# Kernel optimization log

Hardware: AMD Instinct MI355X
Metric: run time of the kernel (lower is better)

Reference implementation:

```python
import jax, jax.numpy as jnp
import numpy as np

N, M, Z_DIM = 32768, 8192, 64


def setup_inputs() -> dict:
    key = jax.random.key(0)
    kz, ke = jax.random.split(key)
    z = jax.random.normal(kz, (N, Z_DIM), dtype=jnp.float32)
    # torch: e = rand(M, z_dim) * 2 - 1  -> uniform in [-1, 1)
    e = jax.random.uniform(ke, (M, Z_DIM), dtype=jnp.float32, minval=-1.0, maxval=1.0)
    return {"z": z, "e": e}


def reference(z, e):
    # data['z'] = tanh(z)
    zt = jnp.tanh(z)                                   # (N, Z)
    # pairwise squared distance via Gram expansion:
    # ||a - b||^2 = ||a||^2 + ||b||^2 - 2 a.b  (same math as the
    # broadcasted sum((a-b)**2) without the (N, M, Z) intermediate)
    zn = jnp.sum(zt * zt, axis=1)                      # (N,)
    en = jnp.sum(e * e, axis=1)                        # (M,)
    distance = zn[:, None] + en[None, :] - 2.0 * (zt @ e.T)   # (N, M)
    # min over the batch dim N for each sample e, then mean over M
    loss = jnp.mean(jnp.min(distance, axis=0))
    return loss
```

## Files before the change

kernel.cpp:

```cpp
#include <hip/hip_runtime.h>
#include <hip/hip_bf16.h>
#include <math.h>

#define NN 32768
#define MM 8192
#define ZD 64
#define WAVES 4
#define MW 128
#define MBLK (WAVES * MW)
#define NCHUNKS 32
#define CHUNK (NN / NCHUNKS)
#define NROWS 64
#define NITER (CHUNK / NROWS)

typedef __attribute__((ext_vector_type(8))) short bf16x8;
typedef __attribute__((ext_vector_type(4))) float f32x4;

__device__ inline unsigned short f2bf(float f) {
  unsigned u = __float_as_uint(f);
  return (unsigned short)((u + 0x7fffu + ((u >> 16) & 1u)) >> 16);
}
__device__ inline float bf2f(unsigned short h) {
  return __uint_as_float(((unsigned)h) << 16);
}

__global__ __launch_bounds__(256) void prep_z(const float* __restrict__ z,
                                              unsigned short* __restrict__ zb,
                                              float* __restrict__ zn) {
  const int row = blockIdx.x * 32 + (threadIdx.x >> 3);
  const int q = threadIdx.x & 7;
  const size_t base = (size_t)row * ZD + q * 8;
  float4 v0 = *reinterpret_cast<const float4*>(&z[base]);
  float4 v1 = *reinterpret_cast<const float4*>(&z[base + 4]);
  float in[8] = {v0.x, v0.y, v0.z, v0.w, v1.x, v1.y, v1.z, v1.w};
  unsigned short b[8];
  float s = 0.f;
#pragma unroll
  for (int i = 0; i < 8; ++i) {
    b[i] = f2bf(tanhf(in[i]));
    float r = bf2f(b[i]);
    s += r * r;
  }
  *reinterpret_cast<bf16x8*>(&zb[base]) = *reinterpret_cast<bf16x8*>(b);
  s += __shfl_xor(s, 1, 64);
  s += __shfl_xor(s, 2, 64);
  s += __shfl_xor(s, 4, 64);
  if (q == 0) zn[row] = s;
}

__global__ __launch_bounds__(256) void prep_e(const float* __restrict__ e,
                                              unsigned short* __restrict__ eb,
                                              float* __restrict__ en) {
  const int row = blockIdx.x * 32 + (threadIdx.x >> 3);
  const int q = threadIdx.x & 7;
  const size_t base = (size_t)row * ZD + q * 8;
  float4 v0 = *reinterpret_cast<const float4*>(&e[base]);
  float4 v1 = *reinterpret_cast<const float4*>(&e[base + 4]);
  float in[8] = {v0.x, v0.y, v0.z, v0.w, v1.x, v1.y, v1.z, v1.w};
  unsigned short b[8];
  float s = 0.f;
#pragma unroll
  for (int i = 0; i < 8; ++i) {
    unsigned short qb = f2bf(in[i]);
    float r = bf2f(qb);
    s += r * r;
    b[i] = f2bf(-2.f * r);
  }
  *reinterpret_cast<bf16x8*>(&eb[base]) = *reinterpret_cast<bf16x8*>(b);
  s += __shfl_xor(s, 1, 64);
  s += __shfl_xor(s, 2, 64);
  s += __shfl_xor(s, 4, 64);
  if (q == 0) en[row] = s;
}

__global__ __launch_bounds__(256) void min_dist(
    const unsigned short* __restrict__ zb, const unsigned short* __restrict__ eb,
    const float* __restrict__ zn, float* __restrict__ partial) {
  __shared__ __align__(128) unsigned short zlds[2][NROWS * ZD];
  const int lane = threadIdx.x & 63;
  const int wv = threadIdx.x >> 6;
  const int lr = lane & 15;
  const int lg = lane >> 4;
  const int m0 = blockIdx.x * MBLK + wv * MW;
  const int nb0 = blockIdx.y * CHUNK;

  const int srow = lane >> 3;
  const int sslot = (lane & 7) ^ srow;

  bf16x8 bfr[8][2];
#pragma unroll
  for (int t = 0; t < 8; ++t)
#pragma unroll
    for (int h = 0; h < 2; ++h)
      bfr[t][h] = *reinterpret_cast<const bf16x8*>(
          &eb[(size_t)(m0 + t * 16 + lr) * ZD + h * 32 + lg * 8]);

  f32x4 minv[8];
#pragma unroll
  for (int t = 0; t < 8; ++t)
    minv[t] = (f32x4){3.4e38f, 3.4e38f, 3.4e38f, 3.4e38f};

  auto stage = [&](int buf, int nb) {
#pragma unroll
    for (int j = 0; j < 2; ++j) {
      const int i = wv * 2 + j;
      const char* src = (const char*)zb +
          (size_t)(nb + i * 8 + srow) * 128 + (sslot << 4);
      char* dst = (char*)&zlds[buf][0] + i * 1024;
      __builtin_amdgcn_global_load_lds(
          (const __attribute__((address_space(1))) unsigned int*)src,
          (__attribute__((address_space(3))) unsigned int*)dst, 16, 0, 0);
    }
  };

  stage(0, nb0);
  __syncthreads();

  for (int it = 0; it < NITER; ++it) {
    const int buf = it & 1;
    if (it + 1 < NITER) stage(buf ^ 1, nb0 + (it + 1) * NROWS);
    const char* lbase = (const char*)&zlds[buf][0];
#pragma unroll
    for (int s = 0; s < 4; ++s) {
      const int rb = (s * 16 + lr) * 128;
      const int x0 = (lg * 16) ^ ((lr & 7) << 4);
      bf16x8 a0 = *reinterpret_cast<const bf16x8*>(lbase + rb + x0);
      bf16x8 a1 = *reinterpret_cast<const bf16x8*>(lbase + rb + (x0 ^ 64));
      f32x4 znv = *reinterpret_cast<const f32x4*>(
          &zn[nb0 + it * NROWS + s * 16 + lg * 4]);
#pragma unroll
      for (int t = 0; t < 8; ++t) {
        f32x4 acc = __builtin_amdgcn_mfma_f32_16x16x32_bf16(a0, bfr[t][0], znv, 0, 0, 0);
        acc = __builtin_amdgcn_mfma_f32_16x16x32_bf16(a1, bfr[t][1], acc, 0, 0, 0);
#pragma unroll
        for (int r = 0; r < 4; ++r) minv[t][r] = fminf(minv[t][r], acc[r]);
      }
    }
    __syncthreads();
  }

#pragma unroll
  for (int t = 0; t < 8; ++t) {
    float v = fminf(fminf(minv[t][0], minv[t][1]), fminf(minv[t][2], minv[t][3]));
    v = fminf(v, __shfl_xor(v, 16, 64));
    v = fminf(v, __shfl_xor(v, 32, 64));
    if (lg == 0) partial[(size_t)blockIdx.y * MM + m0 + t * 16 + lr] = v;
  }
}

__global__ __launch_bounds__(256) void finalize1(const float* __restrict__ partial,
                                                 const float* __restrict__ en,
                                                 double* __restrict__ bsum) {
  const int m = blockIdx.x * 256 + threadIdx.x;
  float mv = partial[m];
#pragma unroll
  for (int c = 1; c < NCHUNKS; ++c)
    mv = fminf(mv, partial[(size_t)c * MM + m]);
  double s = (double)(mv + en[m]);
  __shared__ double sred[256];
  sred[threadIdx.x] = s;
  __syncthreads();
  for (int off = 128; off > 0; off >>= 1) {
    if ((int)threadIdx.x < off) sred[threadIdx.x] += sred[threadIdx.x + off];
    __syncthreads();
  }
  if (threadIdx.x == 0) bsum[blockIdx.x] = sred[0];
}

__global__ __launch_bounds__(64) void finalize2(const double* __restrict__ bsum,
                                                float* __restrict__ out) {
  double s = (threadIdx.x < MM / 256) ? bsum[threadIdx.x] : 0.0;
  s += __shfl_xor(s, 1, 64);
  s += __shfl_xor(s, 2, 64);
  s += __shfl_xor(s, 4, 64);
  s += __shfl_xor(s, 8, 64);
  s += __shfl_xor(s, 16, 64);
  s += __shfl_xor(s, 32, 64);
  if (threadIdx.x == 0) out[0] = (float)(s / (double)MM);
}

extern "C" void kernel_launch(void* const* d_in, const int* in_sizes, int n_in,
                              void* d_out, int out_size, void* d_ws, size_t ws_size,
                              hipStream_t stream) {
  const float* z = (const float*)d_in[0];
  const float* e = (const float*)d_in[1];
  float* out = (float*)d_out;

  unsigned short* zb = (unsigned short*)d_ws;
  unsigned short* eb = zb + (size_t)NN * ZD;
  float* zn = (float*)(eb + (size_t)MM * ZD);
  float* en = zn + NN;
  float* partial = en + MM;
  double* bsum = (double*)(partial + (size_t)NCHUNKS * MM);

  prep_z<<<NN / 32, 256, 0, stream>>>(z, zb, zn);
  prep_e<<<MM / 32, 256, 0, stream>>>(e, eb, en);
  dim3 grid(MM / MBLK, NCHUNKS);
  min_dist<<<grid, 256, 0, stream>>>(zb, eb, zn, partial);
  finalize1<<<MM / 256, 256, 0, stream>>>(partial, en, bsum);
  finalize2<<<1, 64, 0, stream>>>(bsum, out);
}
```

Baseline: 55.25 us.

## Halve per-wave M tile, remap 1D grid across XCDs, add occupancy hint

Each wave now covers 64 columns of e instead of 128, so the grid doubles to 1024 workgroups with fewer registers per wave, and launch_bounds requests 4 blocks per CU. The 2D grid becomes 1D with a swizzle that spreads consecutive block IDs across the 8 XCDs while keeping same-chunk blocks together for L2 reuse of z. Staging addresses and zn pointers are precomputed and incremented instead of recomputed each iteration. The cost is that each z tile loaded into LDS feeds half as many MFMAs per wave, which doubles LDS staging traffic relative to compute.

```diff
diff --git a/kernel.cpp b/kernel.cpp
--- a/kernel.cpp
+++ b/kernel.cpp
@@ -6,8 +6,9 @@
 #define MM 8192
 #define ZD 64
 #define WAVES 4
-#define MW 128
+#define MW 64
 #define MBLK (WAVES * MW)
+#define NMB (MM / MBLK)
 #define NCHUNKS 32
 #define CHUNK (NN / NCHUNKS)
 #define NROWS 64
@@ -73,78 +74,86 @@
   if (q == 0) en[row] = s;
 }
 
-__global__ __launch_bounds__(256) void min_dist(
+__global__ __launch_bounds__(256, 4) void min_dist(
     const unsigned short* __restrict__ zb, const unsigned short* __restrict__ eb,
     const float* __restrict__ zn, float* __restrict__ partial) {
   __shared__ __align__(128) unsigned short zlds[2][NROWS * ZD];
+  const int wg = ((blockIdx.x & 7) << 7) + (blockIdx.x >> 3);
+  const int mb = wg & (NMB - 1);
+  const int cb = wg >> 5;
   const int lane = threadIdx.x & 63;
   const int wv = threadIdx.x >> 6;
   const int lr = lane & 15;
   const int lg = lane >> 4;
-  const int m0 = blockIdx.x * MBLK + wv * MW;
-  const int nb0 = blockIdx.y * CHUNK;
+  const int m0 = mb * MBLK + wv * MW;
+  const int nb0 = cb * CHUNK;
 
   const int srow = lane >> 3;
   const int sslot = (lane & 7) ^ srow;
-
-  bf16x8 bfr[8][2];
-#pragma unroll
-  for (int t = 0; t < 8; ++t)
+  const char* zsrc = (const char*)zb + (size_t)nb0 * 128 +
+                     (wv * 16 + srow) * 128 + (sslot << 4);
+  char* ldst0 = (char*)&zlds[0][0] + wv * 2048;
+  char* ldst1 = (char*)&zlds[1][0] + wv * 2048;
+
+  bf16x8 bfr[4][2];
+#pragma unroll
+  for (int t = 0; t < 4; ++t)
 #pragma unroll
     for (int h = 0; h < 2; ++h)
       bfr[t][h] = *reinterpret_cast<const bf16x8*>(
           &eb[(size_t)(m0 + t * 16 + lr) * ZD + h * 32 + lg * 8]);
 
-  f32x4 minv[8];
-#pragma unroll
-  for (int t = 0; t < 8; ++t)
+  f32x4 minv[4];
+#pragma unroll
+  for (int t = 0; t < 4; ++t)
     minv[t] = (f32x4){3.4e38f, 3.4e38f, 3.4e38f, 3.4e38f};
 
-  auto stage = [&](int buf, int nb) {
-#pragma unroll
-    for (int j = 0; j < 2; ++j) {
-      const int i = wv * 2 + j;
-      const char* src = (const char*)zb +
-          (size_t)(nb + i * 8 + srow) * 128 + (sslot << 4);
-      char* dst = (char*)&zlds[buf][0] + i * 1024;
-      __builtin_amdgcn_global_load_lds(
-          (const __attribute__((address_space(1))) unsigned int*)src,
-          (__attribute__((address_space(3))) unsigned int*)dst, 16, 0, 0);
+  auto stage = [&](char* dst, const char* src) {
+    __builtin_amdgcn_global_load_lds(
+        (const __attribute__((address_space(1))) unsigned int*)src,
+        (__attribute__((address_space(3))) unsigned int*)dst, 16, 0, 0);
+    __builtin_amdgcn_global_load_lds(
+        (const __attribute__((address_space(1))) unsigned int*)(src + 1024),
+        (__attribute__((address_space(3))) unsigned int*)(dst + 1024), 16, 0, 0);
+  };
+
+  const float* znp = zn + nb0;
+  const int x0 = (lg * 16) ^ ((lr & 7) << 4);
+
+  stage(ldst0, zsrc);
+  zsrc += 8192;
+  __syncthreads();
+
+  for (int it = 0; it < NITER; ++it) {
+    const char* lbase = (it & 1) ? (const char*)&zlds[1][0] : (const char*)&zlds[0][0];
+    if (it + 1 < NITER) {
+      stage((it & 1) ? ldst0 : ldst1, zsrc);
+      zsrc += 8192;
     }
-  };
-
-  stage(0, nb0);
-  __syncthreads();
-
-  for (int it = 0; it < NITER; ++it) {
-    const int buf = it & 1;
-    if (it + 1 < NITER) stage(buf ^ 1, nb0 + (it + 1) * NROWS);
-    const char* lbase = (const char*)&zlds[buf][0];
 #pragma unroll
     for (int s = 0; s < 4; ++s) {
       const int rb = (s * 16 + lr) * 128;
-      const int x0 = (lg * 16) ^ ((lr & 7) << 4);
       bf16x8 a0 = *reinterpret_cast<const bf16x8*>(lbase + rb + x0);
       bf16x8 a1 = *reinterpret_cast<const bf16x8*>(lbase + rb + (x0 ^ 64));
-      f32x4 znv = *reinterpret_cast<const f32x4*>(
-          &zn[nb0 + it * NROWS + s * 16 + lg * 4]);
-#pragma unroll
-      for (int t = 0; t < 8; ++t) {
+      f32x4 znv = *reinterpret_cast<const f32x4*>(znp + s * 16 + lg * 4);
+#pragma unroll
+      for (int t = 0; t < 4; ++t) {
         f32x4 acc = __builtin_amdgcn_mfma_f32_16x16x32_bf16(a0, bfr[t][0], znv, 0, 0, 0);
         acc = __builtin_amdgcn_mfma_f32_16x16x32_bf16(a1, bfr[t][1], acc, 0, 0, 0);
 #pragma unroll
         for (int r = 0; r < 4; ++r) minv[t][r] = fminf(minv[t][r], acc[r]);
       }
     }
+    znp += NROWS;
     __syncthreads();
   }
 
 #pragma unroll
-  for (int t = 0; t < 8; ++t) {
+  for (int t = 0; t < 4; ++t) {
     float v = fminf(fminf(minv[t][0], minv[t][1]), fminf(minv[t][2], minv[t][3]));
     v = fminf(v, __shfl_xor(v, 16, 64));
     v = fminf(v, __shfl_xor(v, 32, 64));
-    if (lg == 0) partial[(size_t)blockIdx.y * MM + m0 + t * 16 + lr] = v;
+    if (lg == 0) partial[(size_t)cb * MM + m0 + t * 16 + lr] = v;
   }
 }
 
@@ -195,8 +204,7 @@
 
   prep_z<<<NN / 32, 256, 0, stream>>>(z, zb, zn);
   prep_e<<<MM / 32, 256, 0, stream>>>(e, eb, en);
-  dim3 grid(MM / MBLK, NCHUNKS);
-  min_dist<<<grid, 256, 0, stream>>>(zb, eb, zn, partial);
+  min_dist<<<NMB * NCHUNKS, 256, 0, stream>>>(zb, eb, zn, partial);
   finalize1<<<MM / 256, 256, 0, stream>>>(partial, en, bsum);
   finalize2<<<1, 64, 0, stream>>>(bsum, out);
 }
```

New measurement: 49.22 us. -10.9%, faster.
